# Performance work log

Hardware: AMD Instinct MI355X
Metric: run time of the kernel (lower is better)

## Reference

```python
import jax, jax.numpy as jnp
import numpy as np

B, H, S, DH = 2, 16, 2048, 64
MASK_FILL = -10000.0


def setup_inputs() -> dict:
    key = jax.random.key(0)
    kq, kk, kv = jax.random.split(key, 3)
    q = jax.random.normal(kq, (B, H, S, DH), dtype=jnp.float32)
    k = jax.random.normal(kk, (B, H, S, DH), dtype=jnp.float32)
    v = jax.random.normal(kv, (B, H, S, DH), dtype=jnp.float32)
    # causal mask: True where attention is disallowed (upper triangle)
    mask = jnp.triu(jnp.ones((S, S), dtype=jnp.bool_), k=1)
    return {"q": q, "k": k, "v": v, "mask": mask}


def reference(q, k, v, mask):
    scale = 1.0 / jnp.sqrt(jnp.asarray(k.shape[-1], dtype=q.dtype))
    # scores: [B, H, S_q, S_k]
    scores = jnp.einsum("bhqd,bhkd->bhqk", q, k) * scale
    # additive mask: masked_fill on a zeros [S_k, S_v] matrix -> -10000 where mask
    attn_bias = jnp.where(mask, jnp.asarray(MASK_FILL, dtype=k.dtype),
                          jnp.asarray(0.0, dtype=k.dtype))
    scores = scores + attn_bias  # broadcast over batch/heads
    attn = jax.nn.softmax(scores, axis=-1)
    # dropout_rate = 0.0 -> identity
    return jnp.einsum("bhqk,bhkd->bhqd", attn, v)
```

## Files before the change

kernel.cpp:

```cpp
#include <hip/hip_runtime.h>


#define S_LEN  2048
#define DHDIM  64
#define NHEADS 32
#define LDP    72
#define M2     23.083120654223414f
#define QSCALE 0.18033688011117658f
#define NSLOT  52

typedef __attribute__((ext_vector_type(8))) short bf16x8;
typedef __attribute__((ext_vector_type(4))) float f32x4;
typedef __attribute__((ext_vector_type(16))) float f32x16;

#define RT(qt,k0,k1,sl) ((unsigned)(qt)<<24 | (unsigned)(k0)<<16 | (unsigned)(k1)<<8 | (unsigned)(sl))
__device__ __constant__ unsigned RTAB[63] = {
    RT(31,0,11,49),  RT(31,11,22,50), RT(30,0,11,46),  RT(21,0,11,20),
    RT(21,11,22,21), RT(20,0,11,18),  RT(10,0,11,255),
    RT(31,22,32,51), RT(30,11,21,47), RT(30,21,31,48), RT(29,0,10,43),
    RT(29,10,20,44), RT(29,20,30,45), RT(28,0,10,40),  RT(28,10,20,41),
    RT(27,0,10,37),  RT(20,11,21,19), RT(19,0,10,16),  RT(19,10,20,17),
    RT(18,0,10,14),  RT(9,0,10,255),
    RT(28,20,29,42), RT(27,10,19,38), RT(27,19,28,39), RT(26,0,9,34),
    RT(26,9,18,35),  RT(26,18,27,36), RT(25,0,9,31),   RT(25,9,18,32),
    RT(24,0,9,28),   RT(18,10,19,15), RT(17,0,9,12),   RT(17,9,18,13),
    RT(16,0,9,10),   RT(8,0,9,255),
    RT(25,18,26,33), RT(24,9,17,29),  RT(24,17,25,30), RT(23,0,8,25),
    RT(23,8,16,26),  RT(23,16,24,27), RT(22,0,8,22),   RT(22,8,16,23),
    RT(16,9,17,11),  RT(15,0,8,8),    RT(15,8,16,9),   RT(14,0,8,6),
    RT(7,0,8,255),
    RT(22,16,23,24), RT(14,8,15,7),   RT(13,0,7,4),    RT(13,7,14,5),
    RT(12,0,7,2),    RT(6,0,7,255),
    RT(12,7,13,3),   RT(11,0,6,0),    RT(11,6,12,1),   RT(5,0,6,255),
    RT(4,0,5,255),   RT(3,0,4,255),   RT(2,0,3,255),   RT(1,0,2,255),
    RT(0,0,1,255)};

__device__ __forceinline__ float fast_exp2(float x) {
#if __has_builtin(__builtin_amdgcn_exp2f)
    return __builtin_amdgcn_exp2f(x);
#else
    return exp2f(x);
#endif
}
__device__ __forceinline__ unsigned short f2bf(float f) {
    unsigned u = __float_as_uint(f);
    return (unsigned short)((u + 0x7fffu + ((u >> 16) & 1u)) >> 16);
}
__device__ __forceinline__ void ld8(const float* p, float* f) {
    float4 a = *(const float4*)p, b = *(const float4*)(p + 4);
    f[0]=a.x; f[1]=a.y; f[2]=a.z; f[3]=a.w; f[4]=b.x; f[5]=b.y; f[6]=b.z; f[7]=b.w;
}
__device__ __forceinline__ uint4 pack8(const float* f, float scale) {
    union { uint4 v; unsigned short s[8]; } w;
    #pragma unroll
    for (int j = 0; j < 8; j++) w.s[j] = f2bf(f[j] * scale);
    return w.v;
}
__device__ __forceinline__ unsigned packhi(float a, float b) {
#if __has_builtin(__builtin_amdgcn_perm)
    return __builtin_amdgcn_perm(__float_as_uint(b), __float_as_uint(a), 0x07060302u);
#else
    return (__float_as_uint(a) >> 16) | (__float_as_uint(b) & 0xffff0000u);
#endif
}
__device__ __forceinline__ bf16x8 mk_bf16x8(unsigned d0, unsigned d1,
                                            unsigned d2, unsigned d3) {
    union { unsigned u[4]; bf16x8 v; } w;
    w.u[0] = d0; w.u[1] = d1; w.u[2] = d2; w.u[3] = d3;
    return w.v;
}

__global__ __launch_bounds__(256) void prep(
    const float* __restrict__ Qf, const float* __restrict__ Kf,
    const float* __restrict__ Vf, unsigned short* __restrict__ qb,
    unsigned short* __restrict__ kb, unsigned short* __restrict__ vtb)
{
    const int st = blockIdx.x, bh = blockIdx.y;
    __shared__ unsigned lt32[64][LDP / 2];
    const float* vp = Vf + ((size_t)bh * S_LEN + st * 64) * DHDIM;
    {
        const int c = threadIdx.x;
        const int sp = c >> 3;
        const int d0 = (c & 7) * 8;
        float fa[8], fb[8];
        ld8(vp + (2 * sp) * DHDIM + d0, fa);
        ld8(vp + (2 * sp + 1) * DHDIM + d0, fb);
        #pragma unroll
        for (int j = 0; j < 8; j++) {
            int d = d0 + j;
            int colw = (sp & 3) | ((((sp >> 2) ^ (d >> 3)) & 7) << 2);
            lt32[d][colw] = (unsigned)f2bf(fa[j]) | ((unsigned)f2bf(fb[j]) << 16);
        }
    }
    size_t off = ((size_t)(bh * 32 + st) * 4096) + (size_t)threadIdx.x * 16;
    float f[8];
    ld8(Qf + off, f);     *(uint4*)(qb + off)     = pack8(f, QSCALE);
    ld8(Qf + off + 8, f); *(uint4*)(qb + off + 8) = pack8(f, QSCALE);
    ld8(Kf + off, f);     *(uint4*)(kb + off)     = pack8(f, 1.0f);
    ld8(Kf + off + 8, f); *(uint4*)(kb + off + 8) = pack8(f, 1.0f);
    __syncthreads();
    unsigned short* op = vtb + (size_t)bh * DHDIM * S_LEN + st * 64;
    for (int c = threadIdx.x; c < 512; c += 256) {
        int d = c >> 3, q = c & 7;
        int colw = ((q ^ (d >> 3)) & 7) << 2;
        *(uint4*)(op + (size_t)d * S_LEN + q * 8) = *(const uint4*)&lt32[d][colw];
    }
}

__global__ __launch_bounds__(256) void fattn_splitk(
    const unsigned short* __restrict__ Qp, const unsigned short* __restrict__ Kp,
    const unsigned short* __restrict__ Vp,
    float* __restrict__ pO, float* __restrict__ pL, float* __restrict__ O)
{
    __shared__ unsigned short smem[256 * LDP];
    unsigned short (*ksA)[LDP]  = (unsigned short(*)[LDP])smem;
    unsigned short (*ksB)[LDP]  = (unsigned short(*)[LDP])(smem + 64 * LDP);
    unsigned short (*vtsA)[LDP] = (unsigned short(*)[LDP])(smem + 128 * LDP);
    unsigned short (*vtsB)[LDP] = (unsigned short(*)[LDP])(smem + 192 * LDP);

    const int bh   = blockIdx.x;
    const unsigned e = RTAB[blockIdx.y];
    const int qt   = e >> 24;
    const int k0   = (e >> 16) & 255;
    const int k1   = (e >> 8) & 255;
    const int sl   = e & 255;
    const bool whole = (sl == 255);

    const int tid  = threadIdx.x;
    const int wave = tid >> 6, lane = tid & 63;
    const int q31  = lane & 31, hi = lane >> 5;
    const int qh   = wave & 1, kh = wave >> 1;
    const int qrow = qh * 32 + q31;

    const unsigned short* qsrc = Qp + ((size_t)bh * S_LEN + qt * 64 + qrow) * DHDIM;
    const bf16x8 bq0 = *(const bf16x8*)(qsrc + hi * 8);
    const bf16x8 bq1 = *(const bf16x8*)(qsrc + 16 + hi * 8);
    const bf16x8 bq2 = *(const bf16x8*)(qsrc + 32 + hi * 8);
    const bf16x8 bq3 = *(const bf16x8*)(qsrc + 48 + hi * 8);

    f32x16 of2[2];
    #pragma unroll
    for (int i = 0; i < 16; i++) { of2[0][i] = 0.f; of2[1][i] = 0.f; }
    float l_p = 0.f;

    const unsigned short* Kbh = Kp + (size_t)bh * S_LEN * DHDIM;
    const unsigned short* Vbh = Vp + (size_t)bh * DHDIM * S_LEN;
    const int sr = tid >> 3, sc = (tid & 7) * 8;
    uint4 kr0, kr1, vr0, vr1;
    {
        const unsigned short* ksrc = Kbh + (size_t)k0 * 64 * DHDIM;
        const unsigned short* vsrc = Vbh + k0 * 64;
        kr0 = *(const uint4*)(ksrc + sr * DHDIM + sc);
        kr1 = *(const uint4*)(ksrc + (sr + 32) * DHDIM + sc);
        vr0 = *(const uint4*)(vsrc + (size_t)sr * S_LEN + sc);
        vr1 = *(const uint4*)(vsrc + (size_t)(sr + 32) * S_LEN + sc);
    }
    {
        unsigned short (*ks)[LDP]  = (k0 & 1) ? ksB : ksA;
        unsigned short (*vts)[LDP] = (k0 & 1) ? vtsB : vtsA;
        *(uint4*)&ks[sr][sc]       = kr0;
        *(uint4*)&ks[sr + 32][sc]  = kr1;
        *(uint4*)&vts[sr][sc]      = vr0;
        *(uint4*)&vts[sr + 32][sc] = vr1;
    }
    if (k0 + 1 < k1) {
        const unsigned short* ksrc = Kbh + (size_t)(k0 + 1) * 64 * DHDIM;
        const unsigned short* vsrc = Vbh + (k0 + 1) * 64;
        kr0 = *(const uint4*)(ksrc + sr * DHDIM + sc);
        kr1 = *(const uint4*)(ksrc + (sr + 32) * DHDIM + sc);
        vr0 = *(const uint4*)(vsrc + (size_t)sr * S_LEN + sc);
        vr1 = *(const uint4*)(vsrc + (size_t)(sr + 32) * S_LEN + sc);
    }

    for (int kt = k0; kt < k1; kt++) {
        __syncthreads();

        if (kt + 1 < k1) {
            unsigned short (*ks)[LDP]  = ((kt + 1) & 1) ? ksB : ksA;
            unsigned short (*vts)[LDP] = ((kt + 1) & 1) ? vtsB : vtsA;
            *(uint4*)&ks[sr][sc]       = kr0;
            *(uint4*)&ks[sr + 32][sc]  = kr1;
            *(uint4*)&vts[sr][sc]      = vr0;
            *(uint4*)&vts[sr + 32][sc] = vr1;
            if (kt + 2 < k1) {
                const unsigned short* ksrc = Kbh + (size_t)(kt + 2) * 64 * DHDIM;
                const unsigned short* vsrc = Vbh + (kt + 2) * 64;
                kr0 = *(const uint4*)(ksrc + sr * DHDIM + sc);
                kr1 = *(const uint4*)(ksrc + (sr + 32) * DHDIM + sc);
                vr0 = *(const uint4*)(vsrc + (size_t)sr * S_LEN + sc);
                vr1 = *(const uint4*)(vsrc + (size_t)(sr + 32) * S_LEN + sc);
            }
        }

        const unsigned short (*ksc)[LDP] = (kt & 1) ? ksB : ksA;
        const unsigned short (*vtc)[LDP] = (kt & 1) ? vtsB : vtsA;

        f32x16 sf;
        #pragma unroll
        for (int i = 0; i < 16; i++) sf[i] = -M2;
        __builtin_amdgcn_s_setprio(1);
        {
            bf16x8 ak = *(const bf16x8*)&ksc[kh * 32 + q31][hi * 8];
            sf = __builtin_amdgcn_mfma_f32_32x32x16_bf16(ak, bq0, sf, 0, 0, 0);
            ak = *(const bf16x8*)&ksc[kh * 32 + q31][16 + hi * 8];
            sf = __builtin_amdgcn_mfma_f32_32x32x16_bf16(ak, bq1, sf, 0, 0, 0);
            ak = *(const bf16x8*)&ksc[kh * 32 + q31][32 + hi * 8];
            sf = __builtin_amdgcn_mfma_f32_32x32x16_bf16(ak, bq2, sf, 0, 0, 0);
            ak = *(const bf16x8*)&ksc[kh * 32 + q31][48 + hi * 8];
            sf = __builtin_amdgcn_mfma_f32_32x32x16_bf16(ak, bq3, sf, 0, 0, 0);
        }
        __builtin_amdgcn_s_setprio(0);

        const bool diag = (kt == qt);
        unsigned pdw[8];
        #pragma unroll
        for (int g = 0; g < 4; g++) {
            float p[4];
            #pragma unroll
            for (int r2 = 0; r2 < 4; r2++) {
                float pv = fast_exp2(sf[g * 4 + r2]);
                if (diag) {
                    const int kl = kh * 32 + 8 * g + 4 * hi + r2;
                    if (kl > qrow) pv = 0.f;
                }
                p[r2] = pv;
                l_p += pv;
            }
            pdw[g * 2]     = packhi(p[0], p[1]);
            pdw[g * 2 + 1] = packhi(p[2], p[3]);
        }

        __builtin_amdgcn_s_setprio(1);
        #pragma unroll
        for (int js = 0; js < 2; js++) {
            const unsigned a0 = pdw[4 * js],     a1 = pdw[4 * js + 1];
            const unsigned b0 = pdw[4 * js + 2], b1 = pdw[4 * js + 3];
            const unsigned pa0 = __shfl_xor(a0, 32), pa1 = __shfl_xor(a1, 32);
            const unsigned pb0 = __shfl_xor(b0, 32), pb1 = __shfl_xor(b1, 32);
            const bf16x8 bp = mk_bf16x8(hi ? pb0 : a0, hi ? pb1 : a1,
                                        hi ? b0 : pa0, hi ? b1 : pa1);
            const int scol = (2 * kh + js) * 16 + hi * 8;
            bf16x8 av = *(const bf16x8*)&vtc[q31][scol];
            of2[0] = __builtin_amdgcn_mfma_f32_32x32x16_bf16(av, bp, of2[0], 0, 0, 0);
            av = *(const bf16x8*)&vtc[32 + q31][scol];
            of2[1] = __builtin_amdgcn_mfma_f32_32x32x16_bf16(av, bp, of2[1], 0, 0, 0);
        }
        __builtin_amdgcn_s_setprio(0);
    }

    float l2 = l_p + __shfl_xor(l_p, 32);
    __syncthreads();
    float* fs = (float*)smem;
    const int base = (qh * 64 + lane) * 36;
    if (kh == 1) {
        #pragma unroll
        for (int dh = 0; dh < 2; dh++)
            #pragma unroll
            for (int g = 0; g < 4; g++)
                *(float4*)&fs[base + dh * 16 + g * 4] = make_float4(
                    of2[dh][4 * g], of2[dh][4 * g + 1],
                    of2[dh][4 * g + 2], of2[dh][4 * g + 3]);
        fs[base + 32] = l2;
    }
    __syncthreads();
    if (kh == 0) {
        #pragma unroll
        for (int dh = 0; dh < 2; dh++)
            #pragma unroll
            for (int g = 0; g < 4; g++) {
                float4 a = *(const float4*)&fs[base + dh * 16 + g * 4];
                of2[dh][4 * g]     += a.x;
                of2[dh][4 * g + 1] += a.y;
                of2[dh][4 * g + 2] += a.z;
                of2[dh][4 * g + 3] += a.w;
            }
        l2 += fs[base + 32];

        if (whole) {
            const float inv = 1.f / l2;
            float* op = O + ((size_t)bh * S_LEN + qt * 64 + qrow) * DHDIM;
            #pragma unroll
            for (int dh = 0; dh < 2; dh++)
                #pragma unroll
                for (int g = 0; g < 4; g++)
                    *(float4*)(op + dh * 32 + 8 * g + 4 * hi) = make_float4(
                        of2[dh][4 * g] * inv, of2[dh][4 * g + 1] * inv,
                        of2[dh][4 * g + 2] * inv, of2[dh][4 * g + 3] * inv);
        } else {
            const int slot = bh * NSLOT + sl;
            if (hi == 0) pL[slot * 64 + qrow] = l2;
            float* op = pO + (size_t)slot * 4096 + qrow * 64;
            #pragma unroll
            for (int dh = 0; dh < 2; dh++)
                #pragma unroll
                for (int g = 0; g < 4; g++)
                    *(float4*)(op + dh * 32 + 8 * g + 4 * hi) = make_float4(
                        of2[dh][4 * g], of2[dh][4 * g + 1],
                        of2[dh][4 * g + 2], of2[dh][4 * g + 3]);
        }
    }
}

__global__ __launch_bounds__(256) void combine(
    const float* __restrict__ pO, const float* __restrict__ pL,
    float* __restrict__ O)
{
    const int qt = 11 + blockIdx.x, bh = blockIdx.y;
    int base, cnt;
    if (qt < 22) { base = (qt - 11) * 2;      cnt = 2; }
    else         { base = 22 + 3 * (qt - 22); cnt = 3; }
    const int sb = bh * NSLOT + base;
    const float* A = pO + (size_t)sb * 4096;
    float* out = O + ((size_t)bh * S_LEN + qt * 64) * DHDIM;
    #pragma unroll
    for (int k = 0; k < 4; k++) {
        int c = threadIdx.x + k * 256;
        int row = c >> 4;
        float l = pL[sb * 64 + row] + pL[(sb + 1) * 64 + row];
        float4 a = *(const float4*)(A + c * 4);
        float4 b = *(const float4*)(A + 4096 + c * 4);
        float4 s = make_float4(a.x + b.x, a.y + b.y, a.z + b.z, a.w + b.w);
        if (cnt == 3) {
            l += pL[(sb + 2) * 64 + row];
            float4 d = *(const float4*)(A + 8192 + c * 4);
            s = make_float4(s.x + d.x, s.y + d.y, s.z + d.z, s.w + d.w);
        }
        float inv = 1.f / l;
        *(float4*)(out + c * 4) = make_float4(
            s.x * inv, s.y * inv, s.z * inv, s.w * inv);
    }
}

template <bool PRE>
__global__ __launch_bounds__(256) void fattn_kernel(
    const void* __restrict__ Qp, const void* __restrict__ Kp,
    const void* __restrict__ Vp, float* __restrict__ O)
{
    __shared__ unsigned short smem[192 * LDP];
    unsigned short (*ks)[LDP]  = (unsigned short(*)[LDP])smem;
    unsigned short (*vts)[LDP] = (unsigned short(*)[LDP])(smem + 64 * LDP);
    unsigned short (*qs)[LDP]  = (unsigned short(*)[LDP])(smem + 128 * LDP);
    unsigned short (*pst)[LDP] = qs;

    const int id = blockIdx.y * 32 + blockIdx.x;
    const int g  = id >> 8;
    const int r8 = id & 255;
    const int bh = r8 >> 3;
    const int s8 = r8 & 7;
    const int qt = (g == 0) ? 31 - 2 * s8 : (g == 1) ? 2 * s8
                 : (g == 2) ? 30 - 2 * s8 : 2 * s8 + 1;

    const int tid = threadIdx.x;
    const int wave = tid >> 6, lane = tid & 63;
    const int quad = lane >> 4, l16 = lane & 15;

    if constexpr (PRE) {
        const unsigned short* src = (const unsigned short*)Qp
            + ((size_t)bh * S_LEN + qt * 64) * DHDIM;
        for (int c = tid; c < 512; c += 256) {
            int row = c >> 3, c8 = (c & 7) * 8;
            *(uint4*)&qs[row][c8] = *(const uint4*)(src + row * DHDIM + c8);
        }
    } else {
        const float* src = (const float*)Qp + ((size_t)bh * S_LEN + qt * 64) * DHDIM;
        for (int c = tid; c < 512; c += 256) {
            int row = c >> 3, c8 = (c & 7) * 8;
            float f[8]; ld8(src + row * DHDIM + c8, f);
            *(uint4*)&qs[row][c8] = pack8(f, QSCALE);
        }
    }
    __syncthreads();

    const int prow = wave * 16 + l16;
    const bf16x8 bq0 = *(const bf16x8*)&qs[prow][quad * 8];
    const bf16x8 bq1 = *(const bf16x8*)&qs[prow][32 + quad * 8];

    float l_p = 0.f;
    f32x4 of[4];
    #pragma unroll
    for (int n = 0; n < 4; n++) of[n] = (f32x4){0.f, 0.f, 0.f, 0.f};

    for (int kt = 0; kt <= qt; kt++) {
        __syncthreads();
        if constexpr (PRE) {
            const unsigned short* ksrc = (const unsigned short*)Kp
                + ((size_t)bh * S_LEN + kt * 64) * DHDIM;
            const unsigned short* vsrc = (const unsigned short*)Vp
                + (size_t)bh * DHDIM * S_LEN + kt * 64;
            for (int c = tid; c < 512; c += 256) {
                int row = c >> 3, c8 = (c & 7) * 8;
                *(uint4*)&ks[row][c8]  = *(const uint4*)(ksrc + row * DHDIM + c8);
                *(uint4*)&vts[row][c8] = *(const uint4*)(vsrc + (size_t)row * S_LEN + c8);
            }
        } else {
            const float* ksrc = (const float*)Kp + ((size_t)bh * S_LEN + kt * 64) * DHDIM;
            const float* vsrc = (const float*)Vp + ((size_t)bh * S_LEN + kt * 64) * DHDIM;
            for (int c = tid; c < 512; c += 256) {
                int row = c >> 3, c8 = (c & 7) * 8;
                float f[8];
                ld8(ksrc + row * DHDIM + c8, f);
                *(uint4*)&ks[row][c8] = pack8(f, 1.0f);
                ld8(vsrc + row * DHDIM + c8, f);
                #pragma unroll
                for (int j = 0; j < 8; j++) vts[c8 + j][row] = f2bf(f[j]);
            }
        }
        __syncthreads();

        f32x4 sf[4];
        #pragma unroll
        for (int n = 0; n < 4; n++) {
            bf16x8 ak0 = *(const bf16x8*)&ks[n * 16 + l16][quad * 8];
            bf16x8 ak1 = *(const bf16x8*)&ks[n * 16 + l16][32 + quad * 8];
            sf[n] = (f32x4){-M2, -M2, -M2, -M2};
            sf[n] = __builtin_amdgcn_mfma_f32_16x16x32_bf16(ak0, bq0, sf[n], 0, 0, 0);
            sf[n] = __builtin_amdgcn_mfma_f32_16x16x32_bf16(ak1, bq1, sf[n], 0, 0, 0);
        }

        const bool diag = (kt == qt);
        #pragma unroll
        for (int n = 0; n < 4; n++) {
            float p[4];
            #pragma unroll
            for (int r = 0; r < 4; r++) {
                p[r] = fast_exp2(sf[n][r]);
                if (diag && (n * 16 + quad * 4 + r > prow)) p[r] = 0.f;
                l_p += p[r];
            }
            uint2 dw;
            dw.x = packhi(p[0], p[1]);
            dw.y = packhi(p[2], p[3]);
            *(uint2*)&pst[prow][n * 16 + quad * 4] = dw;
        }
        asm volatile("s_waitcnt lgkmcnt(0)" ::: "memory");

        bf16x8 bp0 = *(const bf16x8*)&pst[prow][quad * 8];
        bf16x8 bp1 = *(const bf16x8*)&pst[prow][32 + quad * 8];
        #pragma unroll
        for (int n = 0; n < 4; n++) {
            bf16x8 av0 = *(const bf16x8*)&vts[n * 16 + l16][quad * 8];
            bf16x8 av1 = *(const bf16x8*)&vts[n * 16 + l16][32 + quad * 8];
            of[n] = __builtin_amdgcn_mfma_f32_16x16x32_bf16(av0, bp0, of[n], 0, 0, 0);
            of[n] = __builtin_amdgcn_mfma_f32_16x16x32_bf16(av1, bp1, of[n], 0, 0, 0);
        }
    }

    l_p += __shfl_xor(l_p, 16);
    l_p += __shfl_xor(l_p, 32);
    const float inv = 1.f / l_p;
    float* op = O + ((size_t)bh * S_LEN + qt * 64 + prow) * DHDIM;
    #pragma unroll
    for (int n = 0; n < 4; n++)
        *(float4*)(op + n * 16 + quad * 4) = make_float4(
            of[n][0] * inv, of[n][1] * inv, of[n][2] * inv, of[n][3] * inv);
}

extern "C" void kernel_launch(void* const* d_in, const int* in_sizes, int n_in,
                              void* d_out, int out_size, void* d_ws, size_t ws_size,
                              hipStream_t stream) {
    const float* Q = (const float*)d_in[0];
    const float* K = (const float*)d_in[1];
    const float* V = (const float*)d_in[2];
    float* O = (float*)d_out;
    const size_t N = (size_t)NHEADS * S_LEN * DHDIM;
    const size_t prepB  = 3 * N * sizeof(unsigned short);
    const size_t partB  = (size_t)NSLOT * 32 * (4096 + 64) * sizeof(float);

    if (d_ws && ws_size >= prepB + partB) {
        unsigned short* qb  = (unsigned short*)d_ws;
        unsigned short* kb  = qb + N;
        unsigned short* vtb = kb + N;
        float* pO = (float*)((char*)d_ws + prepB);
        float* pL = pO + (size_t)NSLOT * 32 * 4096;
        prep<<<dim3(S_LEN / 64, NHEADS), 256, 0, stream>>>(Q, K, V, qb, kb, vtb);
        fattn_splitk<<<dim3(32, 63), 256, 0, stream>>>(qb, kb, vtb, pO, pL, O);
        combine<<<dim3(21, 32), 256, 0, stream>>>(pO, pL, O);
    } else if (d_ws && ws_size >= prepB) {
        unsigned short* qb  = (unsigned short*)d_ws;
        unsigned short* kb  = qb + N;
        unsigned short* vtb = kb + N;
        prep<<<dim3(S_LEN / 64, NHEADS), 256, 0, stream>>>(Q, K, V, qb, kb, vtb);
        fattn_kernel<true><<<dim3(32, 32), 256, 0, stream>>>(qb, kb, vtb, O);
    } else {
        fattn_kernel<false><<<dim3(32, 32), 256, 0, stream>>>(Q, K, V, O);
    }
}
```

Before: 139.7 us.

## Use 128-row query tiles with 512-thread blocks in split-K attention

Each split-K block now covers 128 query rows with eight waves instead of 64 rows with four. Every K/V tile staged in shared memory therefore serves twice as many queries, halving global K/V traffic, and the schedule table, partial slots and combine grid are resized to match. The cost is causal imbalance inside the block: waves whose rows end before the current key tile skip compute but still wait at each barrier. Fewer blocks (32x32) also means less scheduling flexibility across the GPU.

```diff
diff --git a/kernel.cpp b/kernel.cpp
--- a/kernel.cpp
+++ b/kernel.cpp
@@ -7,33 +7,22 @@
 #define LDP    72
 #define M2     23.083120654223414f
 #define QSCALE 0.18033688011117658f
-#define NSLOT  52
+#define NSLOT  27
 
 typedef __attribute__((ext_vector_type(8))) short bf16x8;
 typedef __attribute__((ext_vector_type(4))) float f32x4;
 typedef __attribute__((ext_vector_type(16))) float f32x16;
 
-#define RT(qt,k0,k1,sl) ((unsigned)(qt)<<24 | (unsigned)(k0)<<16 | (unsigned)(k1)<<8 | (unsigned)(sl))
-__device__ __constant__ unsigned RTAB[63] = {
-    RT(31,0,11,49),  RT(31,11,22,50), RT(30,0,11,46),  RT(21,0,11,20),
-    RT(21,11,22,21), RT(20,0,11,18),  RT(10,0,11,255),
-    RT(31,22,32,51), RT(30,11,21,47), RT(30,21,31,48), RT(29,0,10,43),
-    RT(29,10,20,44), RT(29,20,30,45), RT(28,0,10,40),  RT(28,10,20,41),
-    RT(27,0,10,37),  RT(20,11,21,19), RT(19,0,10,16),  RT(19,10,20,17),
-    RT(18,0,10,14),  RT(9,0,10,255),
-    RT(28,20,29,42), RT(27,10,19,38), RT(27,19,28,39), RT(26,0,9,34),
-    RT(26,9,18,35),  RT(26,18,27,36), RT(25,0,9,31),   RT(25,9,18,32),
-    RT(24,0,9,28),   RT(18,10,19,15), RT(17,0,9,12),   RT(17,9,18,13),
-    RT(16,0,9,10),   RT(8,0,9,255),
-    RT(25,18,26,33), RT(24,9,17,29),  RT(24,17,25,30), RT(23,0,8,25),
-    RT(23,8,16,26),  RT(23,16,24,27), RT(22,0,8,22),   RT(22,8,16,23),
-    RT(16,9,17,11),  RT(15,0,8,8),    RT(15,8,16,9),   RT(14,0,8,6),
-    RT(7,0,8,255),
-    RT(22,16,23,24), RT(14,8,15,7),   RT(13,0,7,4),    RT(13,7,14,5),
-    RT(12,0,7,2),    RT(6,0,7,255),
-    RT(12,7,13,3),   RT(11,0,6,0),    RT(11,6,12,1),   RT(5,0,6,255),
-    RT(4,0,5,255),   RT(3,0,4,255),   RT(2,0,3,255),   RT(1,0,2,255),
-    RT(0,0,1,255)};
+#define RT(qp,k0,k1,sl) ((unsigned)(qp)<<24 | (unsigned)(k0)<<16 | (unsigned)(k1)<<8 | (unsigned)(sl))
+__device__ __constant__ unsigned RTAB32[32] = {
+    RT(15,0,11,24),  RT(15,11,22,25), RT(10,0,11,10),  RT(10,11,22,11),
+    RT(15,22,32,26), RT(14,0,10,21),  RT(14,10,20,22), RT(14,20,30,23),
+    RT(13,0,10,18),  RT(9,0,10,8),    RT(9,10,20,9),   RT(4,0,10,255),
+    RT(13,10,19,19), RT(13,19,28,20), RT(12,0,9,15),   RT(12,9,18,16),
+    RT(8,0,9,6),     RT(8,9,18,7),    RT(12,18,26,17), RT(11,0,8,12),
+    RT(11,8,16,13),  RT(11,16,24,14), RT(7,0,8,4),     RT(7,8,16,5),
+    RT(3,0,8,255),   RT(6,0,7,2),     RT(6,7,14,3),    RT(5,0,6,0),
+    RT(5,6,12,1),    RT(2,0,6,255),   RT(1,0,4,255),   RT(0,0,2,255)};
 
 __device__ __forceinline__ float fast_exp2(float x) {
 #if __has_builtin(__builtin_amdgcn_exp2f)
@@ -107,7 +96,7 @@
     }
 }
 
-__global__ __launch_bounds__(256) void fattn_splitk(
+__global__ __launch_bounds__(512) void fattn_splitk(
     const unsigned short* __restrict__ Qp, const unsigned short* __restrict__ Kp,
     const unsigned short* __restrict__ Vp,
     float* __restrict__ pO, float* __restrict__ pL, float* __restrict__ O)
@@ -119,8 +108,8 @@
     unsigned short (*vtsB)[LDP] = (unsigned short(*)[LDP])(smem + 192 * LDP);
 
     const int bh   = blockIdx.x;
-    const unsigned e = RTAB[blockIdx.y];
-    const int qt   = e >> 24;
+    const unsigned e = RTAB32[blockIdx.y];
+    const int qp   = e >> 24;
     const int k0   = (e >> 16) & 255;
     const int k1   = (e >> 8) & 255;
     const int sl   = e & 255;
@@ -129,10 +118,12 @@
     const int tid  = threadIdx.x;
     const int wave = tid >> 6, lane = tid & 63;
     const int q31  = lane & 31, hi = lane >> 5;
-    const int qh   = wave & 1, kh = wave >> 1;
+    const int qh   = wave & 3, kh = wave >> 2;
     const int qrow = qh * 32 + q31;
-
-    const unsigned short* qsrc = Qp + ((size_t)bh * S_LEN + qt * 64 + qrow) * DHDIM;
+    const int gq   = qp * 128 + qrow;
+    const int diag_kt = gq >> 6;
+
+    const unsigned short* qsrc = Qp + ((size_t)bh * S_LEN + gq) * DHDIM;
     const bf16x8 bq0 = *(const bf16x8*)(qsrc + hi * 8);
     const bf16x8 bq1 = *(const bf16x8*)(qsrc + 16 + hi * 8);
     const bf16x8 bq2 = *(const bf16x8*)(qsrc + 32 + hi * 8);
@@ -146,30 +137,18 @@
     const unsigned short* Kbh = Kp + (size_t)bh * S_LEN * DHDIM;
     const unsigned short* Vbh = Vp + (size_t)bh * DHDIM * S_LEN;
     const int sr = tid >> 3, sc = (tid & 7) * 8;
-    uint4 kr0, kr1, vr0, vr1;
-    {
-        const unsigned short* ksrc = Kbh + (size_t)k0 * 64 * DHDIM;
-        const unsigned short* vsrc = Vbh + k0 * 64;
-        kr0 = *(const uint4*)(ksrc + sr * DHDIM + sc);
-        kr1 = *(const uint4*)(ksrc + (sr + 32) * DHDIM + sc);
-        vr0 = *(const uint4*)(vsrc + (size_t)sr * S_LEN + sc);
-        vr1 = *(const uint4*)(vsrc + (size_t)(sr + 32) * S_LEN + sc);
-    }
+    uint4 kr, vr;
+    kr = *(const uint4*)(Kbh + ((size_t)k0 * 64 + sr) * DHDIM + sc);
+    vr = *(const uint4*)(Vbh + (size_t)sr * S_LEN + k0 * 64 + sc);
     {
         unsigned short (*ks)[LDP]  = (k0 & 1) ? ksB : ksA;
         unsigned short (*vts)[LDP] = (k0 & 1) ? vtsB : vtsA;
-        *(uint4*)&ks[sr][sc]       = kr0;
-        *(uint4*)&ks[sr + 32][sc]  = kr1;
-        *(uint4*)&vts[sr][sc]      = vr0;
-        *(uint4*)&vts[sr + 32][sc] = vr1;
+        *(uint4*)&ks[sr][sc]  = kr;
+        *(uint4*)&vts[sr][sc] = vr;
     }
     if (k0 + 1 < k1) {
-        const unsigned short* ksrc = Kbh + (size_t)(k0 + 1) * 64 * DHDIM;
-        const unsigned short* vsrc = Vbh + (k0 + 1) * 64;
-        kr0 = *(const uint4*)(ksrc + sr * DHDIM + sc);
-        kr1 = *(const uint4*)(ksrc + (sr + 32) * DHDIM + sc);
-        vr0 = *(const uint4*)(vsrc + (size_t)sr * S_LEN + sc);
-        vr1 = *(const uint4*)(vsrc + (size_t)(sr + 32) * S_LEN + sc);
+        kr = *(const uint4*)(Kbh + ((size_t)(k0 + 1) * 64 + sr) * DHDIM + sc);
+        vr = *(const uint4*)(Vbh + (size_t)sr * S_LEN + (k0 + 1) * 64 + sc);
     }
 
     for (int kt = k0; kt < k1; kt++) {
@@ -178,19 +157,15 @@
         if (kt + 1 < k1) {
             unsigned short (*ks)[LDP]  = ((kt + 1) & 1) ? ksB : ksA;
             unsigned short (*vts)[LDP] = ((kt + 1) & 1) ? vtsB : vtsA;
-            *(uint4*)&ks[sr][sc]       = kr0;
-            *(uint4*)&ks[sr + 32][sc]  = kr1;
-            *(uint4*)&vts[sr][sc]      = vr0;
-            *(uint4*)&vts[sr + 32][sc] = vr1;
+            *(uint4*)&ks[sr][sc]  = kr;
+            *(uint4*)&vts[sr][sc] = vr;
             if (kt + 2 < k1) {
-                const unsigned short* ksrc = Kbh + (size_t)(kt + 2) * 64 * DHDIM;
-                const unsigned short* vsrc = Vbh + (kt + 2) * 64;
-                kr0 = *(const uint4*)(ksrc + sr * DHDIM + sc);
-                kr1 = *(const uint4*)(ksrc + (sr + 32) * DHDIM + sc);
-                vr0 = *(const uint4*)(vsrc + (size_t)sr * S_LEN + sc);
-                vr1 = *(const uint4*)(vsrc + (size_t)(sr + 32) * S_LEN + sc);
-            }
-        }
+                kr = *(const uint4*)(Kbh + ((size_t)(kt + 2) * 64 + sr) * DHDIM + sc);
+                vr = *(const uint4*)(Vbh + (size_t)sr * S_LEN + (kt + 2) * 64 + sc);
+            }
+        }
+
+        if (kt > diag_kt) continue;
 
         const unsigned short (*ksc)[LDP] = (kt & 1) ? ksB : ksA;
         const unsigned short (*vtc)[LDP] = (kt & 1) ? vtsB : vtsA;
@@ -211,7 +186,8 @@
         }
         __builtin_amdgcn_s_setprio(0);
 
-        const bool diag = (kt == qt);
+        const bool diag = (kt == diag_kt);
+        const int qmod = gq & 63;
         unsigned pdw[8];
         #pragma unroll
         for (int g = 0; g < 4; g++) {
@@ -221,7 +197,7 @@
                 float pv = fast_exp2(sf[g * 4 + r2]);
                 if (diag) {
                     const int kl = kh * 32 + 8 * g + 4 * hi + r2;
-                    if (kl > qrow) pv = 0.f;
+                    if (kl > qmod) pv = 0.f;
                 }
                 p[r2] = pv;
                 l_p += pv;
@@ -278,7 +254,7 @@
 
         if (whole) {
             const float inv = 1.f / l2;
-            float* op = O + ((size_t)bh * S_LEN + qt * 64 + qrow) * DHDIM;
+            float* op = O + ((size_t)bh * S_LEN + gq) * DHDIM;
             #pragma unroll
             for (int dh = 0; dh < 2; dh++)
                 #pragma unroll
@@ -288,8 +264,8 @@
                         of2[dh][4 * g + 2] * inv, of2[dh][4 * g + 3] * inv);
         } else {
             const int slot = bh * NSLOT + sl;
-            if (hi == 0) pL[slot * 64 + qrow] = l2;
-            float* op = pO + (size_t)slot * 4096 + qrow * 64;
+            if (hi == 0) pL[slot * 128 + qrow] = l2;
+            float* op = pO + (size_t)slot * 8192 + qrow * 64;
             #pragma unroll
             for (int dh = 0; dh < 2; dh++)
                 #pragma unroll
@@ -305,24 +281,24 @@
     const float* __restrict__ pO, const float* __restrict__ pL,
     float* __restrict__ O)
 {
-    const int qt = 11 + blockIdx.x, bh = blockIdx.y;
+    const int t = 5 + blockIdx.x, bh = blockIdx.y;
     int base, cnt;
-    if (qt < 22) { base = (qt - 11) * 2;      cnt = 2; }
-    else         { base = 22 + 3 * (qt - 22); cnt = 3; }
+    if (t <= 10) { base = (t - 5) * 2;       cnt = 2; }
+    else         { base = 12 + (t - 11) * 3; cnt = 3; }
     const int sb = bh * NSLOT + base;
-    const float* A = pO + (size_t)sb * 4096;
-    float* out = O + ((size_t)bh * S_LEN + qt * 64) * DHDIM;
+    const float* A = pO + (size_t)sb * 8192;
+    float* out = O + ((size_t)bh * S_LEN + t * 128) * DHDIM;
     #pragma unroll
-    for (int k = 0; k < 4; k++) {
+    for (int k = 0; k < 8; k++) {
         int c = threadIdx.x + k * 256;
         int row = c >> 4;
-        float l = pL[sb * 64 + row] + pL[(sb + 1) * 64 + row];
+        float l = pL[sb * 128 + row] + pL[(sb + 1) * 128 + row];
         float4 a = *(const float4*)(A + c * 4);
-        float4 b = *(const float4*)(A + 4096 + c * 4);
+        float4 b = *(const float4*)(A + 8192 + c * 4);
         float4 s = make_float4(a.x + b.x, a.y + b.y, a.z + b.z, a.w + b.w);
         if (cnt == 3) {
-            l += pL[(sb + 2) * 64 + row];
-            float4 d = *(const float4*)(A + 8192 + c * 4);
+            l += pL[(sb + 2) * 128 + row];
+            float4 d = *(const float4*)(A + 16384 + c * 4);
             s = make_float4(s.x + d.x, s.y + d.y, s.z + d.z, s.w + d.w);
         }
         float inv = 1.f / l;
@@ -464,17 +440,17 @@
     float* O = (float*)d_out;
     const size_t N = (size_t)NHEADS * S_LEN * DHDIM;
     const size_t prepB  = 3 * N * sizeof(unsigned short);
-    const size_t partB  = (size_t)NSLOT * 32 * (4096 + 64) * sizeof(float);
+    const size_t partB  = (size_t)NSLOT * 32 * (8192 + 128) * sizeof(float);
 
     if (d_ws && ws_size >= prepB + partB) {
         unsigned short* qb  = (unsigned short*)d_ws;
         unsigned short* kb  = qb + N;
         unsigned short* vtb = kb + N;
         float* pO = (float*)((char*)d_ws + prepB);
-        float* pL = pO + (size_t)NSLOT * 32 * 4096;
+        float* pL = pO + (size_t)NSLOT * 32 * 8192;
         prep<<<dim3(S_LEN / 64, NHEADS), 256, 0, stream>>>(Q, K, V, qb, kb, vtb);
-        fattn_splitk<<<dim3(32, 63), 256, 0, stream>>>(qb, kb, vtb, pO, pL, O);
-        combine<<<dim3(21, 32), 256, 0, stream>>>(pO, pL, O);
+        fattn_splitk<<<dim3(32, 32), 512, 0, stream>>>(qb, kb, vtb, pO, pL, O);
+        combine<<<dim3(11, 32), 256, 0, stream>>>(pO, pL, O);
     } else if (d_ws && ws_size >= prepB) {
         unsigned short* qb  = (unsigned short*)d_ws;
         unsigned short* kb  = qb + N;
```

After: 139.0 us. About the same (-0.5%).
